# Kernel tuning notes

Hardware: AMD Instinct MI355X
Metric: run time of the kernel (lower is better)

## Reference

```python
import jax, jax.numpy as jnp
import numpy as np

N_VOX = 200000   # active input voxels
M_VOX = 100000   # active output voxels
K_VOL = 27       # 3x3x3 kernel offsets
C_IN = 32
C_OUT = 64


def setup_inputs() -> dict:
    key = jax.random.key(0)
    k1, k2, k3, k4 = jax.random.split(key, 4)
    feats = jax.random.normal(k1, (N_VOX, C_IN), dtype=jnp.float32)
    # kernel init ~ U(-std, std), std = 1/sqrt(in_channels * kernel_volume)
    std = 1.0 / np.sqrt(C_IN * K_VOL)
    kernel = jax.random.uniform(k2, (K_VOL, C_IN, C_OUT), dtype=jnp.float32,
                                minval=-std, maxval=std)
    # kernel map: for each offset k and output voxel m, an input voxel index
    in_idx = jax.random.randint(k3, (K_VOL, M_VOX), 0, N_VOX, dtype=jnp.int32)
    # occupancy mask: 1 if that (offset, output) pair exists in the kernel map
    mask = jax.random.randint(k4, (K_VOL, M_VOX), 0, 2, dtype=jnp.int32)
    return {"feats": feats, "kernel": kernel, "in_idx": in_idx, "mask": mask}


def reference(feats, kernel, in_idx, mask) -> jnp.ndarray:
    # Gather neighbor features per kernel offset: [K, M, C_in]
    gathered = feats[in_idx]
    gathered = gathered * mask[..., None].astype(feats.dtype)
    # Per-offset GEMM + scatter-add (offsets align on output voxels, so the
    # scatter-add is a sum over the K axis): [M, C_out]
    out = jnp.einsum('kmi,kio->mo', gathered, kernel)
    return out
```

## Files before the change

kernel.cpp:

```cpp
#include <hip/hip_runtime.h>

#define M_VOX   100000
#define N_VOX   200000
#define K_VOL   27
#define C_IN    32
#define C_OUT   64

#define STG0        14
#define BLK_THREADS 1024
#define VOX_PER_BLK 256

typedef __bf16 bf16x8 __attribute__((ext_vector_type(8)));
typedef float  floatx4 __attribute__((ext_vector_type(4)));

#define FEATSB_BYTES  ((N_VOX + 1) * C_IN * 2)
#define BFRAG_OFF     FEATSB_BYTES

#define FEAT_CHUNKS   ((N_VOX + 1) * 4)
#define FEAT_BLOCKS   ((FEAT_CHUNKS + 255) / 256)
__global__ __launch_bounds__(256) void prep_all(
    const float* __restrict__ feats, const float* __restrict__ kernelw,
    __bf16* __restrict__ featsB, bf16x8* __restrict__ Bfrag)
{
    if (blockIdx.x < FEAT_BLOCKS) {
        const int c = blockIdx.x * 256 + threadIdx.x;
        if (c >= FEAT_CHUNKS) return;
        bf16x8 v;
        if (c < N_VOX * 4) {
            floatx4 f0 = *(const floatx4*)(feats + c * 8);
            floatx4 f1 = *(const floatx4*)(feats + c * 8 + 4);
#pragma unroll
            for (int j = 0; j < 4; ++j) { v[j] = (__bf16)f0[j]; v[4 + j] = (__bf16)f1[j]; }
        } else {
#pragma unroll
            for (int j = 0; j < 8; ++j) v[j] = (__bf16)0.0f;
        }
        *(bf16x8*)(featsB + c * 8) = v;
    } else {
        const int k    = blockIdx.x - FEAT_BLOCKS;
        const int tid  = threadIdx.x;
        const int tile = tid >> 6;
        const int col  = tid & 15;
        const int quad = (tid >> 4) & 3;
        const float* kp = kernelw + k * C_IN * C_OUT + quad * 8 * C_OUT + tile * 16 + col;
        bf16x8 b;
#pragma unroll
        for (int j = 0; j < 8; ++j) b[j] = (__bf16)kp[j * C_OUT];
        Bfrag[k * 256 + tid] = b;
    }
}

__global__ __launch_bounds__(BLK_THREADS) void sparse_conv_mfma(
    const __bf16* __restrict__ featsB,
    const bf16x8* __restrict__ BfragG,
    const int* __restrict__ in_idx,
    const int* __restrict__ mask,
    float* __restrict__ out)
{
    __shared__ bf16x8 ldsB[STG0 * 256];

    const int tid  = threadIdx.x;
    const int lane = tid & 63;
    const int wv   = tid >> 6;
    const int col  = lane & 15;
    const int quad = lane >> 4;

    const int m0 = blockIdx.x * VOX_PER_BLK + wv * 16;
    const bool active = (m0 < M_VOX);

#pragma unroll 2
    for (int i = tid; i < STG0 * 256; i += BLK_THREADS) ldsB[i] = BfragG[i];

    int mi[K_VOL];
    if (active) {
#pragma unroll
        for (int k = 0; k < K_VOL; ++k) {
            const int ix = in_idx[k * M_VOX + m0 + col];
            const int mk = mask[k * M_VOX + m0 + col];
            mi[k] = mk ? ix : N_VOX;
        }
    }
    __syncthreads();

    floatx4 acc0 = {0.f,0.f,0.f,0.f}, acc1 = {0.f,0.f,0.f,0.f};
    floatx4 acc2 = {0.f,0.f,0.f,0.f}, acc3 = {0.f,0.f,0.f,0.f};

    const __bf16*  fbase = featsB + quad * 8;
    const bf16x8*  lbase = ldsB + lane;

    bf16x8 a_n;
    if (active) a_n = *(const bf16x8*)(fbase + (size_t)mi[0] * C_IN);

    if (active) {
#pragma unroll
        for (int k = 0; k < STG0; ++k) {
            bf16x8 a  = a_n;
            bf16x8 b0 = lbase[k * 256 + 0 * 64];
            bf16x8 b1 = lbase[k * 256 + 1 * 64];
            bf16x8 b2 = lbase[k * 256 + 2 * 64];
            bf16x8 b3 = lbase[k * 256 + 3 * 64];
            if (k + 1 < K_VOL)
                a_n = *(const bf16x8*)(fbase + (size_t)mi[k + 1] * C_IN);
            acc0 = __builtin_amdgcn_mfma_f32_16x16x32_bf16(a, b0, acc0, 0, 0, 0);
            acc1 = __builtin_amdgcn_mfma_f32_16x16x32_bf16(a, b1, acc1, 0, 0, 0);
            acc2 = __builtin_amdgcn_mfma_f32_16x16x32_bf16(a, b2, acc2, 0, 0, 0);
            acc3 = __builtin_amdgcn_mfma_f32_16x16x32_bf16(a, b3, acc3, 0, 0, 0);
        }
    }

    __syncthreads();
#pragma unroll 2
    for (int i = tid; i < (K_VOL - STG0) * 256; i += BLK_THREADS)
        ldsB[i] = BfragG[STG0 * 256 + i];
    __syncthreads();

    if (active) {
#pragma unroll
        for (int k = STG0; k < K_VOL; ++k) {
            bf16x8 a  = a_n;
            bf16x8 b0 = lbase[(k - STG0) * 256 + 0 * 64];
            bf16x8 b1 = lbase[(k - STG0) * 256 + 1 * 64];
            bf16x8 b2 = lbase[(k - STG0) * 256 + 2 * 64];
            bf16x8 b3 = lbase[(k - STG0) * 256 + 3 * 64];
            if (k + 1 < K_VOL)
                a_n = *(const bf16x8*)(fbase + (size_t)mi[k + 1] * C_IN);
            acc0 = __builtin_amdgcn_mfma_f32_16x16x32_bf16(a, b0, acc0, 0, 0, 0);
            acc1 = __builtin_amdgcn_mfma_f32_16x16x32_bf16(a, b1, acc1, 0, 0, 0);
            acc2 = __builtin_amdgcn_mfma_f32_16x16x32_bf16(a, b2, acc2, 0, 0, 0);
            acc3 = __builtin_amdgcn_mfma_f32_16x16x32_bf16(a, b3, acc3, 0, 0, 0);
        }

        float* op = out + (size_t)(m0 + quad * 4) * C_OUT + col;
#pragma unroll
        for (int r = 0; r < 4; ++r) {
            op[r * C_OUT + 0]  = acc0[r];
            op[r * C_OUT + 16] = acc1[r];
            op[r * C_OUT + 32] = acc2[r];
            op[r * C_OUT + 48] = acc3[r];
        }
    }
}

extern "C" void kernel_launch(void* const* d_in, const int* in_sizes, int n_in,
                              void* d_out, int out_size, void* d_ws, size_t ws_size,
                              hipStream_t stream) {
    const float* feats   = (const float*)d_in[0];
    const float* kernelw = (const float*)d_in[1];
    const int*   in_idx  = (const int*)d_in[2];
    const int*   maskp   = (const int*)d_in[3];
    float*       out     = (float*)d_out;

    __bf16* featsB = (__bf16*)d_ws;
    bf16x8* BfragP = (bf16x8*)((char*)d_ws + BFRAG_OFF);

    prep_all<<<dim3(FEAT_BLOCKS + K_VOL), dim3(256), 0, stream>>>(
        feats, kernelw, featsB, BfragP);

    const int blocks = (M_VOX + VOX_PER_BLK - 1) / VOX_PER_BLK;
    sparse_conv_mfma<<<dim3(blocks), dim3(BLK_THREADS), 0, stream>>>(
        featsB, BfragP, in_idx, maskp, out);
}
```

Measured before the change: 122.1 us.

## Switch to 32x32x16 MFMA tiles with batched gathers and 512-thread blocks

Replaces the per-wave 16-voxel tile using four 16x16x32 MFMAs with a 32-voxel tile using 32x32x16 bf16 MFMAs and two accumulators. The B fragments are re-laid out in the prep kernel to match. Feature-row gathers are now issued in bursts of five offsets, loading both halves of each row before the MFMAs, to raise memory-level parallelism. The block shrinks to 512 threads (8 waves × 32 voxels), which increases register pressure per wave and changes occupancy.

New measurement: 127.1 us. 1.04x slower.

```diff
diff --git a/kernel.cpp b/kernel.cpp
--- a/kernel.cpp
+++ b/kernel.cpp
@@ -7,11 +7,14 @@
 #define C_OUT   64
 
 #define STG0        14
-#define BLK_THREADS 1024
+#define STG1        (K_VOL - STG0)
+#define BLK_THREADS 512
 #define VOX_PER_BLK 256
+#define BURST       5
 
 typedef __bf16 bf16x8 __attribute__((ext_vector_type(8)));
-typedef float  floatx4 __attribute__((ext_vector_type(4)));
+typedef float  floatx4  __attribute__((ext_vector_type(4)));
+typedef float  floatx16 __attribute__((ext_vector_type(16)));
 
 #define FEATSB_BYTES  ((N_VOX + 1) * C_IN * 2)
 #define BFRAG_OFF     FEATSB_BYTES
@@ -39,10 +42,14 @@
     } else {
         const int k    = blockIdx.x - FEAT_BLOCKS;
         const int tid  = threadIdx.x;
-        const int tile = tid >> 6;
-        const int col  = tid & 15;
-        const int quad = (tid >> 4) & 3;
-        const float* kp = kernelw + k * C_IN * C_OUT + quad * 8 * C_OUT + tile * 16 + col;
+        const int frag = tid >> 6;
+        const int lane = tid & 63;
+        const int h    = frag >> 1;
+        const int t    = frag & 1;
+        const int c32  = lane & 31;
+        const int half = lane >> 5;
+        const float* kp = kernelw + k * C_IN * C_OUT
+                        + (h * 16 + half * 8) * C_OUT + t * 32 + c32;
         bf16x8 b;
 #pragma unroll
         for (int j = 0; j < 8; ++j) b[j] = (__bf16)kp[j * C_OUT];
@@ -62,83 +69,83 @@
     const int tid  = threadIdx.x;
     const int lane = tid & 63;
     const int wv   = tid >> 6;
-    const int col  = lane & 15;
-    const int quad = lane >> 4;
+    const int c32  = lane & 31;
+    const int half = lane >> 5;
 
-    const int m0 = blockIdx.x * VOX_PER_BLK + wv * 16;
+    const int m0 = blockIdx.x * VOX_PER_BLK + wv * 32;
     const bool active = (m0 < M_VOX);
 
-#pragma unroll 2
+#pragma unroll
     for (int i = tid; i < STG0 * 256; i += BLK_THREADS) ldsB[i] = BfragG[i];
 
     int mi[K_VOL];
     if (active) {
 #pragma unroll
         for (int k = 0; k < K_VOL; ++k) {
-            const int ix = in_idx[k * M_VOX + m0 + col];
-            const int mk = mask[k * M_VOX + m0 + col];
+            const int ix = in_idx[k * M_VOX + m0 + c32];
+            const int mk = mask[k * M_VOX + m0 + c32];
             mi[k] = mk ? ix : N_VOX;
         }
     }
     __syncthreads();
 
-    floatx4 acc0 = {0.f,0.f,0.f,0.f}, acc1 = {0.f,0.f,0.f,0.f};
-    floatx4 acc2 = {0.f,0.f,0.f,0.f}, acc3 = {0.f,0.f,0.f,0.f};
+    floatx16 accT0 = {0.f}, accT1 = {0.f};
+#pragma unroll
+    for (int i = 0; i < 16; ++i) { accT0[i] = 0.f; accT1[i] = 0.f; }
 
-    const __bf16*  fbase = featsB + quad * 8;
-    const bf16x8*  lbase = ldsB + lane;
+    const bf16x8* lbase = ldsB + lane;
+    const __bf16* fbase = featsB + half * 8;
 
-    bf16x8 a_n;
-    if (active) a_n = *(const bf16x8*)(fbase + (size_t)mi[0] * C_IN);
+    bf16x8 A0[BURST], A1[BURST];
+
+#define GATHER_BATCH(KB, NB, LOFF)                                            \
+    {                                                                          \
+        _Pragma("unroll")                                                      \
+        for (int j = 0; j < (NB); ++j) {                                       \
+            const __bf16* rp = fbase + (size_t)mi[(KB) + j] * C_IN;            \
+            A0[j] = *(const bf16x8*)(rp);                                      \
+            A1[j] = *(const bf16x8*)(rp + 16);                                 \
+        }                                                                      \
+        _Pragma("unroll")                                                      \
+        for (int j = 0; j < (NB); ++j) {                                       \
+            const int kl = (LOFF) + j;                                         \
+            bf16x8 b00 = lbase[(kl * 4 + 0) * 64];                  \
+            bf16x8 b01 = lbase[(kl * 4 + 1) * 64];                  \
+            bf16x8 b10 = lbase[(kl * 4 + 2) * 64];                  \
+            bf16x8 b11 = lbase[(kl * 4 + 3) * 64];                  \
+            accT0 = __builtin_amdgcn_mfma_f32_32x32x16_bf16(A0[j], b00, accT0, 0, 0, 0); \
+            accT1 = __builtin_amdgcn_mfma_f32_32x32x16_bf16(A0[j], b01, accT1, 0, 0, 0); \
+            accT0 = __builtin_amdgcn_mfma_f32_32x32x16_bf16(A1[j], b10, accT0, 0, 0, 0); \
+            accT1 = __builtin_amdgcn_mfma_f32_32x32x16_bf16(A1[j], b11, accT1, 0, 0, 0); \
+        }                                                                      \
+    }
 
     if (active) {
-#pragma unroll
-        for (int k = 0; k < STG0; ++k) {
-            bf16x8 a  = a_n;
-            bf16x8 b0 = lbase[k * 256 + 0 * 64];
-            bf16x8 b1 = lbase[k * 256 + 1 * 64];
-            bf16x8 b2 = lbase[k * 256 + 2 * 64];
-            bf16x8 b3 = lbase[k * 256 + 3 * 64];
-            if (k + 1 < K_VOL)
-                a_n = *(const bf16x8*)(fbase + (size_t)mi[k + 1] * C_IN);
-            acc0 = __builtin_amdgcn_mfma_f32_16x16x32_bf16(a, b0, acc0, 0, 0, 0);
-            acc1 = __builtin_amdgcn_mfma_f32_16x16x32_bf16(a, b1, acc1, 0, 0, 0);
-            acc2 = __builtin_amdgcn_mfma_f32_16x16x32_bf16(a, b2, acc2, 0, 0, 0);
-            acc3 = __builtin_amdgcn_mfma_f32_16x16x32_bf16(a, b3, acc3, 0, 0, 0);
-        }
+        GATHER_BATCH(0, BURST, 0)
+        GATHER_BATCH(BURST, BURST, BURST)
+        GATHER_BATCH(2 * BURST, STG0 - 2 * BURST, 2 * BURST)
     }
 
     __syncthreads();
-#pragma unroll 2
-    for (int i = tid; i < (K_VOL - STG0) * 256; i += BLK_THREADS)
+#pragma unroll
+    for (int i = tid; i < STG1 * 256; i += BLK_THREADS)
         ldsB[i] = BfragG[STG0 * 256 + i];
     __syncthreads();
 
     if (active) {
+        GATHER_BATCH(STG0, BURST, 0)
+        GATHER_BATCH(STG0 + BURST, BURST, BURST)
+        GATHER_BATCH(STG0 + 2 * BURST, STG1 - 2 * BURST, 2 * BURST)
+
+        float* ob = out + (size_t)m0 * C_OUT + c32;
 #pragma unroll
-        for (int k = STG0; k < K_VOL; ++k) {
-            bf16x8 a  = a_n;
-            bf16x8 b0 = lbase[(k - STG0) * 256 + 0 * 64];
-            bf16x8 b1 = lbase[(k - STG0) * 256 + 1 * 64];
-            bf16x8 b2 = lbase[(k - STG0) * 256 + 2 * 64];
-            bf16x8 b3 = lbase[(k - STG0) * 256 + 3 * 64];
-            if (k + 1 < K_VOL)
-                a_n = *(const bf16x8*)(fbase + (size_t)mi[k + 1] * C_IN);
-            acc0 = __builtin_amdgcn_mfma_f32_16x16x32_bf16(a, b0, acc0, 0, 0, 0);
-            acc1 = __builtin_amdgcn_mfma_f32_16x16x32_bf16(a, b1, acc1, 0, 0, 0);
-            acc2 = __builtin_amdgcn_mfma_f32_16x16x32_bf16(a, b2, acc2, 0, 0, 0);
-            acc3 = __builtin_amdgcn_mfma_f32_16x16x32_bf16(a, b3, acc3, 0, 0, 0);
-        }
-
-        float* op = out + (size_t)(m0 + quad * 4) * C_OUT + col;
-#pragma unroll
-        for (int r = 0; r < 4; ++r) {
-            op[r * C_OUT + 0]  = acc0[r];
-            op[r * C_OUT + 16] = acc1[r];
-            op[r * C_OUT + 32] = acc2[r];
-            op[r * C_OUT + 48] = acc3[r];
+        for (int r = 0; r < 16; ++r) {
+            const int row = (r & 3) + 8 * (r >> 2) + 4 * half;
+            ob[(size_t)row * C_OUT + 0]  = accT0[r];
+            ob[(size_t)row * C_OUT + 32] = accT1[r];
         }
     }
+#undef GATHER_BATCH
 }
 
 extern "C" void kernel_launch(void* const* d_in, const int* in_sizes, int n_in,
```
